# Optimization experiments

Hardware: AMD Instinct MI355X
Metric: run time of the kernel (lower is better)

Reference implementation:

```python
import jax, jax.numpy as jnp
import numpy as np

DIM = 512
HEADS = 8
WIN = 10      # window_size
SHIFT = 5     # shift_size
FRAMES = 1000 # num_frames (N)
HIDDEN = 4 * DIM
EPS = 1e-5


def _layernorm(x, w, b):
    m = jnp.mean(x, axis=-1, keepdims=True)
    v = jnp.mean((x - m) ** 2, axis=-1, keepdims=True)
    return (x - m) * jax.lax.rsqrt(v + EPS) * w + b


def _shift_mask(N):
    pos = jnp.arange(N)
    seg = (pos >= N - WIN).astype(jnp.float32) + (pos >= N - SHIFT).astype(jnp.float32)
    seg = seg.reshape(N // WIN, WIN)
    diff = seg[:, :, None] - seg[:, None, :]
    return jnp.where(diff != 0, -100.0, 0.0)


def setup_inputs() -> dict:
    key = jax.random.key(0)
    ks = jax.random.split(key, 16)
    std = 0.02
    inp = {
        "x": jax.random.normal(ks[0], (64, FRAMES, DIM), dtype=jnp.float32),
        "norm1_w": jnp.ones((DIM,), jnp.float32),
        "norm1_b": jnp.zeros((DIM,), jnp.float32),
        "qkv_w": jax.random.normal(ks[1], (3 * DIM, DIM), jnp.float32) * std,
        "qkv_b": jnp.zeros((3 * DIM,), jnp.float32),
        "rel_bias_table": jax.random.normal(ks[2], (2 * WIN - 1, HEADS), jnp.float32) * std,
        "proj_w": jax.random.normal(ks[3], (DIM, DIM), jnp.float32) * std,
        "proj_b": jnp.zeros((DIM,), jnp.float32),
        "norm2_w": jnp.ones((DIM,), jnp.float32),
        "norm2_b": jnp.zeros((DIM,), jnp.float32),
        "fc1_w": jax.random.normal(ks[4], (HIDDEN, DIM), jnp.float32) * std,
        "fc1_b": jnp.zeros((HIDDEN,), jnp.float32),
        "fc2_w": jax.random.normal(ks[5], (DIM, HIDDEN), jnp.float32) * std,
        "fc2_b": jnp.zeros((DIM,), jnp.float32),
    }
    return inp


def reference(x, norm1_w, norm1_b, qkv_w, qkv_b, rel_bias_table, proj_w, proj_b,
              norm2_w, norm2_b, fc1_w, fc1_b, fc2_w, fc2_b):
    B, N, C = x.shape
    hd = C // HEADS
    scale = hd ** -0.5
    nW = N // WIN

    shortcut = x
    h = _layernorm(x, norm1_w, norm1_b)
    h = jnp.roll(h, -SHIFT, axis=1)                      # cyclic shift
    xw = h.reshape(B * nW, WIN, C)                       # window partition

    qkv = xw @ qkv_w.T + qkv_b
    qkv = qkv.reshape(B * nW, WIN, 3, HEADS, hd).transpose(2, 0, 3, 1, 4)
    q, k, v = qkv[0] * scale, qkv[1], qkv[2]

    attn = jnp.einsum('bhqd,bhkd->bhqk', q, k)
    idx = jnp.arange(WIN)[:, None] - jnp.arange(WIN)[None, :] + WIN - 1
    bias = rel_bias_table[idx]
    attn = attn + bias.transpose(2, 0, 1)[None]

    mask = _shift_mask(N)
    attn = attn.reshape(B, nW, HEADS, WIN, WIN) + mask[None, :, None]
    attn = jax.nn.softmax(attn, axis=-1).reshape(B * nW, HEADS, WIN, WIN)

    out = jnp.einsum('bhqk,bhkd->bhqd', attn, v)
    out = out.transpose(0, 2, 1, 3).reshape(B * nW, WIN, C)
    out = out @ proj_w.T + proj_b

    out = out.reshape(B, N, C)                           # window reverse
    out = jnp.roll(out, SHIFT, axis=1)                   # reverse shift

    x = shortcut + out
    h2 = _layernorm(x, norm2_w, norm2_b)
    h2 = jax.nn.gelu(h2 @ fc1_w.T + fc1_b, approximate=False)
    h2 = h2 @ fc2_w.T + fc2_b
    return x + h2
```

## Files before the change

kernel.cpp:

```cpp
#include <hip/hip_runtime.h>

#define DIMC 512
#define HEADS 8
#define HD 64
#define WINS 10
#define SHIFT_SZ 5
#define FRAMES 1000
#define NWIN 100
#define BATCH 64
#define TOKENS 64000
#define HIDDEN 2048

typedef unsigned short u16;
typedef __attribute__((ext_vector_type(8))) short bf16x8;
typedef __attribute__((ext_vector_type(4))) float f32x4;

__device__ __forceinline__ float bf2f(u16 u) { return __uint_as_float(((unsigned)u) << 16); }
__device__ __forceinline__ u16 f2bf(float f) {
    unsigned u = __float_as_uint(f);
    u += 0x7fffu + ((u >> 16) & 1u);
    return (u16)(u >> 16);
}

__global__ __launch_bounds__(256) void cvt_kernel(const float* __restrict__ src,
                                                  u16* __restrict__ dst, int n) {
    const int i = (blockIdx.x * 256 + threadIdx.x) * 4;
    if (i < n) {
        const float4 v = *(const float4*)(src + i);
        *(ushort4*)(dst + i) = make_ushort4(f2bf(v.x), f2bf(v.y), f2bf(v.z), f2bf(v.w));
    }
}

template <int SH>
__global__ __launch_bounds__(256) void ln_kernel(const float* __restrict__ x,
                                                 const float* __restrict__ w,
                                                 const float* __restrict__ b,
                                                 u16* __restrict__ out) {
    const int wave = threadIdx.x >> 6, lane = threadIdx.x & 63;
    const int row = blockIdx.x * 4 + wave;
    const float4* rp = (const float4*)(x + (size_t)row * DIMC);
    const float4 v0 = rp[lane];
    const float4 v1 = rp[64 + lane];
    float f[8] = {v0.x, v0.y, v0.z, v0.w, v1.x, v1.y, v1.z, v1.w};
    float sum = 0.f, sq = 0.f;
#pragma unroll
    for (int i = 0; i < 8; i++) { sum += f[i]; sq += f[i] * f[i]; }
#pragma unroll
    for (int off = 32; off >= 1; off >>= 1) {
        sum += __shfl_xor(sum, off);
        sq += __shfl_xor(sq, off);
    }
    const float mean = sum * (1.f / DIMC);
    const float var = sq * (1.f / DIMC) - mean * mean;
    const float rstd = rsqrtf(var + 1e-5f);

    const float4 w0 = ((const float4*)w)[lane], w1 = ((const float4*)w)[64 + lane];
    const float4 b0 = ((const float4*)b)[lane], b1 = ((const float4*)b)[64 + lane];
    const float wf[8] = {w0.x, w0.y, w0.z, w0.w, w1.x, w1.y, w1.z, w1.w};
    const float bf[8] = {b0.x, b0.y, b0.z, b0.w, b1.x, b1.y, b1.z, b1.w};
    u16 o[8];
#pragma unroll
    for (int i = 0; i < 8; i++) o[i] = f2bf((f[i] - mean) * rstd * wf[i] + bf[i]);

    int dst = row;
    if (SH) {
        int bb = row / FRAMES;
        int t = row - bb * FRAMES;
        int td = t - SH; if (td < 0) td += FRAMES;
        dst = bb * FRAMES + td;
    }
    u16* op = out + (size_t)dst * DIMC;
    *(ushort4*)(op + 4 * lane) = make_ushort4(o[0], o[1], o[2], o[3]);
    *(ushort4*)(op + 256 + 4 * lane) = make_ushort4(o[4], o[5], o[6], o[7]);
}

__global__ __launch_bounds__(256) void ln_kernel_bf(const u16* __restrict__ x,
                                                    const float* __restrict__ w,
                                                    const float* __restrict__ b,
                                                    u16* __restrict__ out) {
    const int wave = threadIdx.x >> 6, lane = threadIdx.x & 63;
    const int row = blockIdx.x * 4 + wave;
    const uint4 v = ((const uint4*)(x + (size_t)row * DIMC))[lane];
    const unsigned uv[4] = {v.x, v.y, v.z, v.w};
    float f[8];
    float sum = 0.f, sq = 0.f;
#pragma unroll
    for (int i = 0; i < 4; i++) {
        float a = __uint_as_float(uv[i] << 16);
        float c = __uint_as_float(uv[i] & 0xffff0000u);
        f[2 * i] = a; f[2 * i + 1] = c;
        sum += a + c; sq += a * a + c * c;
    }
#pragma unroll
    for (int off = 32; off >= 1; off >>= 1) {
        sum += __shfl_xor(sum, off);
        sq += __shfl_xor(sq, off);
    }
    const float mean = sum * (1.f / DIMC);
    const float var = sq * (1.f / DIMC) - mean * mean;
    const float rstd = rsqrtf(var + 1e-5f);

    const float4 w0 = ((const float4*)w)[2 * lane], w1 = ((const float4*)w)[2 * lane + 1];
    const float4 b0 = ((const float4*)b)[2 * lane], b1 = ((const float4*)b)[2 * lane + 1];
    const float wf[8] = {w0.x, w0.y, w0.z, w0.w, w1.x, w1.y, w1.z, w1.w};
    const float bf[8] = {b0.x, b0.y, b0.z, b0.w, b1.x, b1.y, b1.z, b1.w};
    u16 o[8];
#pragma unroll
    for (int i = 0; i < 8; i++) o[i] = f2bf((f[i] - mean) * rstd * wf[i] + bf[i]);
    uint4 ov;
    ov.x = (unsigned)o[0] | ((unsigned)o[1] << 16);
    ov.y = (unsigned)o[2] | ((unsigned)o[3] << 16);
    ov.z = (unsigned)o[4] | ((unsigned)o[5] << 16);
    ov.w = (unsigned)o[6] | ((unsigned)o[7] << 16);
    ((uint4*)(out + (size_t)row * DIMC))[lane] = ov;
}

#define GLD16(gp, lp)                                                                     \
    __builtin_amdgcn_global_load_lds((const __attribute__((address_space(1))) void*)(gp), \
                                     (__attribute__((address_space(3))) void*)(lp), 16, 0, 0)

template <int MODE>
__global__ __launch_bounds__(256, 2) void gemm_bt(const u16* __restrict__ A,
                                                  const u16* __restrict__ W,
                                                  const float* __restrict__ bias,
                                                  u16* __restrict__ Cb,
                                                  float* __restrict__ Cf,
                                                  const float* __restrict__ Rf,
                                                  const u16* __restrict__ Rb,
                                                  int Nn, int K, int nbn) {
    __shared__ __align__(16) u16 smem[36864];
    const int tid = threadIdx.x;
    const int w = tid >> 6, l = tid & 63;

    const int nwg = gridDim.x;
    const int q8 = nwg >> 3, r8 = nwg & 7;
    const int xcd = blockIdx.x & 7, bidx = blockIdx.x >> 3;
    const int swz = (xcd < r8 ? xcd * (q8 + 1) : r8 * (q8 + 1) + (xcd - r8) * q8) + bidx;
    const int bm = swz / nbn, bn = swz - bm * nbn;

    const int wr = w >> 1, wc = w & 1;
    const int lrow = l & 15, lq = l >> 4;

    f32x4 acc[8][4];
#pragma unroll
    for (int m = 0; m < 8; m++)
#pragma unroll
        for (int n = 0; n < 4; n++) acc[m][n] = (f32x4)0.0f;

    const int gsrc8 = (((tid & 3) ^ ((tid >> 3) & 3)) << 3);
    const u16* Ag = A + (size_t)(bm * 256 + (tid >> 2)) * K + gsrc8;
    const u16* Bg = W + (size_t)(bn * 128 + (tid >> 2)) * K + gsrc8;
    const size_t rowoff = (size_t)64 * K;
    const int lb = w * 512;

#define STAGE(buf, kt) do {                                       \
        u16* sb_ = smem + (buf) * 12288;                          \
        GLD16(Ag + (kt), sb_ + lb);                               \
        GLD16(Ag + rowoff + (kt), sb_ + 2048 + lb);               \
        GLD16(Ag + 2 * rowoff + (kt), sb_ + 4096 + lb);           \
        GLD16(Ag + 3 * rowoff + (kt), sb_ + 6144 + lb);           \
        GLD16(Bg + (kt), sb_ + 8192 + lb);                        \
        GLD16(Bg + rowoff + (kt), sb_ + 10240 + lb);              \
    } while (0)

    const int gran = ((lq ^ ((lrow >> 1) & 3)) << 3);
    const int arow = (wr * 128 + lrow) * 32 + gran;
    const int brow = 8192 + (wc * 64 + lrow) * 32 + gran;

#define COMPUTE(buf) do {                                                          \
        const u16* sb = smem + (buf) * 12288;                                      \
        bf16x8 bv[4];                                                              \
        _Pragma("unroll")                                                          \
        for (int n = 0; n < 4; n++) bv[n] = *(const bf16x8*)(sb + brow + n * 512); \
        _Pragma("unroll")                                                          \
        for (int m = 0; m < 8; m++) {                                              \
            const bf16x8 af = *(const bf16x8*)(sb + arow + m * 512);               \
            _Pragma("unroll")                                                      \
            for (int n = 0; n < 4; n++)              \
                acc[m][n] = __builtin_amdgcn_mfma_f32_16x16x32_bf16(bv[n], af, acc[m][n], 0, 0, 0); \
        }                                                                          \
    } while (0)

    const int nt = K >> 5;
    STAGE(0, 0);
    STAGE(1, 32);
    int cb = 0;
    for (int t = 0; t < nt - 1; ++t) {
        asm volatile("s_waitcnt vmcnt(6)" ::: "memory");
        __builtin_amdgcn_s_barrier();
        __builtin_amdgcn_sched_barrier(0);
        COMPUTE(cb);
        if (t + 2 < nt) {
            const int sbuf = cb == 0 ? 2 : cb - 1;
            STAGE(sbuf, (t + 2) * 32);
        }
        cb = cb == 2 ? 0 : cb + 1;
    }
    asm volatile("s_waitcnt vmcnt(0)" ::: "memory");
    __builtin_amdgcn_s_barrier();
    __builtin_amdgcn_sched_barrier(0);
    COMPUTE(cb);

    if (MODE == 0 || MODE == 1 || MODE == 2) {
        __syncthreads();
#pragma unroll
        for (int m = 0; m < 8; m++) {
            const int row = wr * 128 + m * 16 + lrow;
            const int sw = (row & 7) << 3;
#pragma unroll
            for (int n = 0; n < 4; n++) {
                const int col = wc * 64 + n * 16 + lq * 4;
                const float4 b4 = *(const float4*)(bias + bn * 128 + col);
                float v0 = acc[m][n][0] + b4.x, v1 = acc[m][n][1] + b4.y;
                float v2 = acc[m][n][2] + b4.z, v3 = acc[m][n][3] + b4.w;
                if (MODE == 2) {
                    const float g0 = v0 * (0.7978845608f + 0.0356774081f * v0 * v0);
                    const float g1 = v1 * (0.7978845608f + 0.0356774081f * v1 * v1);
                    const float g2 = v2 * (0.7978845608f + 0.0356774081f * v2 * v2);
                    const float g3 = v3 * (0.7978845608f + 0.0356774081f * v3 * v3);
                    v0 /= (1.f + __expf(-2.f * g0)); v1 /= (1.f + __expf(-2.f * g1));
                    v2 /= (1.f + __expf(-2.f * g2)); v3 /= (1.f + __expf(-2.f * g3));
                }
                *(ushort4*)(smem + row * 128 + ((col ^ sw))) =
                    make_ushort4(f2bf(v0), f2bf(v1), f2bf(v2), f2bf(v3));
            }
        }
        __syncthreads();
        const int c8 = lrow * 8;
#pragma unroll
        for (int i = 0; i < 16; i++) {
            const int r = w * 64 + i * 4 + lq;
            const uint4 val = *(const uint4*)(smem + r * 128 + (c8 ^ ((r & 7) << 3)));
            const int grow = bm * 256 + r;
            if (MODE == 1) {
                int bb = grow / FRAMES;
                int tr = grow - bb * FRAMES;
                int td = tr + SHIFT_SZ; if (td >= FRAMES) td -= FRAMES;
                const size_t dr = (size_t)(bb * FRAMES + td) * DIMC + bn * 128 + c8;
                const float4 rA = *(const float4*)(Rf + dr);
                const float4 rB = *(const float4*)(Rf + dr + 4);
                const u16* vp = (const u16*)&val;
                u16 o[8];
                o[0] = f2bf(bf2f(vp[0]) + rA.x); o[1] = f2bf(bf2f(vp[1]) + rA.y);
                o[2] = f2bf(bf2f(vp[2]) + rA.z); o[3] = f2bf(bf2f(vp[3]) + rA.w);
                o[4] = f2bf(bf2f(vp[4]) + rB.x); o[5] = f2bf(bf2f(vp[5]) + rB.y);
                o[6] = f2bf(bf2f(vp[6]) + rB.z); o[7] = f2bf(bf2f(vp[7]) + rB.w);
                uint4 ov;
                ov.x = (unsigned)o[0] | ((unsigned)o[1] << 16);
                ov.y = (unsigned)o[2] | ((unsigned)o[3] << 16);
                ov.z = (unsigned)o[4] | ((unsigned)o[5] << 16);
                ov.w = (unsigned)o[6] | ((unsigned)o[7] << 16);
                *(uint4*)(Cb + dr) = ov;
            } else {
                *(uint4*)(Cb + (size_t)grow * Nn + bn * 128 + c8) = val;
            }
        }
    } else {
#pragma unroll
        for (int m = 0; m < 8; m++) {
            const int grow = bm * 256 + wr * 128 + m * 16 + lrow;
#pragma unroll
            for (int n = 0; n < 4; n++) {
                const int gcb = bn * 128 + wc * 64 + n * 16 + lq * 4;
                const float4 b4 = *(const float4*)(bias + gcb);
                const size_t dr = (size_t)grow * Nn + gcb;
                const ushort4 rb = *(const ushort4*)(Rb + dr);
                float4 o;
                o.x = acc[m][n][0] + b4.x + bf2f(rb.x);
                o.y = acc[m][n][1] + b4.y + bf2f(rb.y);
                o.z = acc[m][n][2] + b4.z + bf2f(rb.z);
                o.w = acc[m][n][3] + b4.w + bf2f(rb.w);
                *(float4*)(Cf + dr) = o;
            }
        }
    }
#undef COMPUTE
#undef STAGE
}

__global__ __launch_bounds__(256) void attn_kernel(const u16* __restrict__ qkv_c,
                                                   const float* __restrict__ relb,
                                                   u16* __restrict__ out,
                                                   int win0) {
    __shared__ __align__(16) u16 kv[WINS * 3 * DIMC];
    __shared__ float S[HEADS][WINS][WINS];
    const int tid = threadIdx.x;
    const int win = win0 + blockIdx.x;
    const u16* src = qkv_c + (size_t)blockIdx.x * (WINS * 3 * DIMC);
    for (int idx = tid * 8; idx < WINS * 3 * DIMC; idx += 2048)
        *(uint4*)(kv + idx) = *(const uint4*)(src + idx);
    __syncthreads();

    const bool lastw = (win % NWIN) == (NWIN - 1);
    for (int e = tid; e < HEADS * WINS * WINS; e += 256) {
        const int hh = e / (WINS * WINS);
        const int rem = e - hh * WINS * WINS;
        const int i = rem / WINS, j = rem - (rem / WINS) * WINS;
        const u16* qp = kv + i * (3 * DIMC) + hh * HD;
        const u16* kp = kv + j * (3 * DIMC) + DIMC + hh * HD;
        float s = 0.f;
#pragma unroll
        for (int c = 0; c < 64; c++) s += bf2f(qp[c]) * bf2f(kp[c]);
        s *= 0.125f;
        s += relb[(i - j + WINS - 1) * HEADS + hh];
        if (lastw && ((i < SHIFT_SZ) != (j < SHIFT_SZ))) s -= 100.f;
        S[hh][i][j] = s;
    }
    __syncthreads();

    if (tid < HEADS * WINS) {
        const int hh = tid / WINS, i = tid - (tid / WINS) * WINS;
        float m = -1e30f;
#pragma unroll
        for (int j = 0; j < WINS; j++) m = fmaxf(m, S[hh][i][j]);
        float e[WINS], sum = 0.f;
#pragma unroll
        for (int j = 0; j < WINS; j++) { e[j] = __expf(S[hh][i][j] - m); sum += e[j]; }
        const float inv = 1.f / sum;
#pragma unroll
        for (int j = 0; j < WINS; j++) S[hh][i][j] = e[j] * inv;
    }
    __syncthreads();

    {
        const int hh = tid >> 5, dl = tid & 31;
#pragma unroll
        for (int half = 0; half < 2; half++) {
            const int d = dl + half * 32;
            float vv[WINS];
#pragma unroll
            for (int j = 0; j < WINS; j++) vv[j] = bf2f(kv[j * (3 * DIMC) + 2 * DIMC + hh * HD + d]);
#pragma unroll
            for (int i = 0; i < WINS; i++) {
                float o = 0.f;
#pragma unroll
                for (int j = 0; j < WINS; j++) o += S[hh][i][j] * vv[j];
                out[(size_t)(win * WINS + i) * DIMC + hh * HD + d] = f2bf(o);
            }
        }
    }
}

extern "C" void kernel_launch(void* const* d_in, const int* in_sizes, int n_in,
                              void* d_out, int out_size, void* d_ws, size_t ws_size,
                              hipStream_t stream) {
    const float* x     = (const float*)d_in[0];
    const float* n1w   = (const float*)d_in[1];
    const float* n1b   = (const float*)d_in[2];
    const float* qkvw  = (const float*)d_in[3];
    const float* qkvb  = (const float*)d_in[4];
    const float* relb  = (const float*)d_in[5];
    const float* projw = (const float*)d_in[6];
    const float* projb = (const float*)d_in[7];
    const float* n2w   = (const float*)d_in[8];
    const float* n2b   = (const float*)d_in[9];
    const float* fc1w  = (const float*)d_in[10];
    const float* fc1b  = (const float*)d_in[11];
    const float* fc2w  = (const float*)d_in[12];
    const float* fc2b  = (const float*)d_in[13];

    float* outp = (float*)d_out;
    char* ws = (char*)d_ws;
    u16* wb_qkv  = (u16*)(ws);
    u16* wb_proj = (u16*)(ws + 1572864);
    u16* wb_fc1  = (u16*)(ws + 2097152);
    u16* wb_fc2  = (u16*)(ws + 4194304);
    u16* r0  = (u16*)(ws + 6291456);
    u16* x2b = (u16*)(ws + 71827456);
    u16* big = (u16*)(ws + 137363456);

    cvt_kernel<<<768, 256, 0, stream>>>(qkvw, wb_qkv, 786432);
    cvt_kernel<<<256, 256, 0, stream>>>(projw, wb_proj, 262144);
    cvt_kernel<<<1024, 256, 0, stream>>>(fc1w, wb_fc1, 1048576);
    cvt_kernel<<<1024, 256, 0, stream>>>(fc2w, wb_fc2, 1048576);

    const size_t avail = ws_size > (size_t)137363456 ? ws_size - (size_t)137363456 : 0;
    const int nc1 = (avail >= (size_t)98304000) ? 2
                  : (avail >= (size_t)39321600) ? 5 : (avail >= (size_t)19660800) ? 10 : 50;
    const int nc2 = (avail >= (size_t)131072000) ? 2
                  : (avail >= (size_t)52428800) ? 5 : (avail >= (size_t)26214400) ? 10 : 25;

    ln_kernel<SHIFT_SZ><<<TOKENS / 4, 256, 0, stream>>>(x, n1w, n1b, r0);

    const int rows1 = TOKENS / nc1;
    for (int c = 0; c < nc1; ++c) {
        const int row0 = c * rows1;
        gemm_bt<0><<<(rows1 / 256) * 12, 256, 0, stream>>>(
            r0 + (size_t)row0 * DIMC, wb_qkv, qkvb, big, nullptr, nullptr, nullptr, 1536, DIMC, 12);
        attn_kernel<<<rows1 / WINS, 256, 0, stream>>>(big, relb, r0, row0 / WINS);
    }

    gemm_bt<1><<<(TOKENS / 256) * 4, 256, 0, stream>>>(
        r0, wb_proj, projb, x2b, nullptr, x, nullptr, DIMC, DIMC, 4);

    ln_kernel_bf<<<TOKENS / 4, 256, 0, stream>>>(x2b, n2w, n2b, r0);

    const int rows2 = TOKENS / nc2;
    for (int c = 0; c < nc2; ++c) {
        const int row0 = c * rows2;
        gemm_bt<2><<<(rows2 / 256) * 16, 256, 0, stream>>>(
            r0 + (size_t)row0 * DIMC, wb_fc1, fc1b, big, nullptr, nullptr, nullptr, HIDDEN, DIMC, 16);
        gemm_bt<3><<<(rows2 / 256) * 4, 256, 0, stream>>>(
            big, wb_fc2, fc2b, nullptr, outp + (size_t)row0 * DIMC, nullptr,
            x2b + (size_t)row0 * DIMC, DIMC, HIDDEN, 4);
    }
}
```

Measured before the change: 767.7 us.

## Replace GEMM with 256x256-tile, 8-wave kernel and split-phase K pipeline

Replaces the 256x128-tile, 4-wave GEMM with a 256x256-tile kernel using 512 threads (8 waves in a 2x4 grid) and a 64-deep K step. The K step is double-buffered and split into four sub-phases, with loads interleaved between MFMA groups and s_setprio raised around the MFMA groups. The larger tile doubles operand reuse per LDS byte and halves redundant A reads. In exchange it uses 128KB of LDS per block, which limits occupancy, and it halves the number of workgroups.

```diff
diff --git a/kernel.cpp b/kernel.cpp
--- a/kernel.cpp
+++ b/kernel.cpp
@@ -120,15 +120,15 @@
                                      (__attribute__((address_space(3))) void*)(lp), 16, 0, 0)
 
 template <int MODE>
-__global__ __launch_bounds__(256, 2) void gemm_bt(const u16* __restrict__ A,
-                                                  const u16* __restrict__ W,
-                                                  const float* __restrict__ bias,
-                                                  u16* __restrict__ Cb,
-                                                  float* __restrict__ Cf,
-                                                  const float* __restrict__ Rf,
-                                                  const u16* __restrict__ Rb,
-                                                  int Nn, int K, int nbn) {
-    __shared__ __align__(16) u16 smem[36864];
+__global__ __launch_bounds__(512, 2) void gemm8(const u16* __restrict__ A,
+                                                const u16* __restrict__ W,
+                                                const float* __restrict__ bias,
+                                                u16* __restrict__ Cb,
+                                                float* __restrict__ Cf,
+                                                const float* __restrict__ Rf,
+                                                const u16* __restrict__ Rb,
+                                                int Nn, int K, int nbn) {
+    __shared__ __align__(16) u16 smem[65536];
     const int tid = threadIdx.x;
     const int w = tid >> 6, l = tid & 63;
 
@@ -138,7 +138,7 @@
     const int swz = (xcd < r8 ? xcd * (q8 + 1) : r8 * (q8 + 1) + (xcd - r8) * q8) + bidx;
     const int bm = swz / nbn, bn = swz - bm * nbn;
 
-    const int wr = w >> 1, wc = w & 1;
+    const int wm = w >> 2, wn = w & 3;
     const int lrow = l & 15, lq = l >> 4;
 
     f32x4 acc[8][4];
@@ -147,70 +147,113 @@
 #pragma unroll
         for (int n = 0; n < 4; n++) acc[m][n] = (f32x4)0.0f;
 
-    const int gsrc8 = (((tid & 3) ^ ((tid >> 3) & 3)) << 3);
-    const u16* Ag = A + (size_t)(bm * 256 + (tid >> 2)) * K + gsrc8;
-    const u16* Bg = W + (size_t)(bn * 128 + (tid >> 2)) * K + gsrc8;
-    const size_t rowoff = (size_t)64 * K;
-    const int lb = w * 512;
-
-#define STAGE(buf, kt) do {                                       \
-        u16* sb_ = smem + (buf) * 12288;                          \
-        GLD16(Ag + (kt), sb_ + lb);                               \
-        GLD16(Ag + rowoff + (kt), sb_ + 2048 + lb);               \
-        GLD16(Ag + 2 * rowoff + (kt), sb_ + 4096 + lb);           \
-        GLD16(Ag + 3 * rowoff + (kt), sb_ + 6144 + lb);           \
-        GLD16(Bg + (kt), sb_ + 8192 + lb);                        \
-        GLD16(Bg + rowoff + (kt), sb_ + 10240 + lb);              \
-    } while (0)
+    const int lgsrc8 = (((tid & 3) ^ ((tid >> 3) & 3)) << 3);
+    const u16* Ag = A + (size_t)(bm * 256 + (tid >> 2)) * K + lgsrc8;
+    const u16* Wg = W + (size_t)(bn * 256 + (tid >> 2)) * K + lgsrc8;
+    const size_t roff = (size_t)128 * K;
+    const int ldsw = w * 512;
+
+#define STG2(base, G, kc) do {                          \
+        GLD16((G) + (kc), smem + (base) + ldsw);        \
+        GLD16((G) + roff + (kc), smem + (base) + 4096 + ldsw); } while (0)
 
     const int gran = ((lq ^ ((lrow >> 1) & 3)) << 3);
-    const int arow = (wr * 128 + lrow) * 32 + gran;
-    const int brow = 8192 + (wc * 64 + lrow) * 32 + gran;
-
-#define COMPUTE(buf) do {                                                          \
-        const u16* sb = smem + (buf) * 12288;                                      \
-        bf16x8 bv[4];                                                              \
-        _Pragma("unroll")                                                          \
-        for (int n = 0; n < 4; n++) bv[n] = *(const bf16x8*)(sb + brow + n * 512); \
-        _Pragma("unroll")                                                          \
-        for (int m = 0; m < 8; m++) {                                              \
-            const bf16x8 af = *(const bf16x8*)(sb + arow + m * 512);               \
-            _Pragma("unroll")                                                      \
-            for (int n = 0; n < 4; n++)              \
-                acc[m][n] = __builtin_amdgcn_mfma_f32_16x16x32_bf16(bv[n], af, acc[m][n], 0, 0, 0); \
-        }                                                                          \
-    } while (0)
-
-    const int nt = K >> 5;
-    STAGE(0, 0);
-    STAGE(1, 32);
-    int cb = 0;
-    for (int t = 0; t < nt - 1; ++t) {
-        asm volatile("s_waitcnt vmcnt(6)" ::: "memory");
+    const int agb = (wm * 128 + lrow) * 32 + gran;
+    const int bgb = (wn * 64 + lrow) * 32 + gran;
+
+    const int NT = K >> 6;
+
+    STG2(0, Ag, 0);
+    STG2(32768, Wg, 0);
+    STG2(8192, Ag, 32);
+    STG2(32768 + 8192, Wg, 32);
+
+    for (int tt = 0; tt < NT; ++tt) {
+        const int buf = tt & 1;
+        const u16* Ab = smem + buf * 16384;
+        const u16* Bb = smem + 32768 + buf * 16384;
+        const int nb = (buf ^ 1) * 16384;
+        const int nk = (tt + 1) << 6;
+        const bool more = (tt + 1) < NT;
+        bf16x8 af[8];
+
+        if (more) STG2(nb, Ag, nk);
+        if (more) asm volatile("s_waitcnt vmcnt(6)" ::: "memory");
+        else      asm volatile("s_waitcnt vmcnt(4)" ::: "memory");
         __builtin_amdgcn_s_barrier();
         __builtin_amdgcn_sched_barrier(0);
-        COMPUTE(cb);
-        if (t + 2 < nt) {
-            const int sbuf = cb == 0 ? 2 : cb - 1;
-            STAGE(sbuf, (t + 2) * 32);
-        }
-        cb = cb == 2 ? 0 : cb + 1;
-    }
-    asm volatile("s_waitcnt vmcnt(0)" ::: "memory");
-    __builtin_amdgcn_s_barrier();
-    __builtin_amdgcn_sched_barrier(0);
-    COMPUTE(cb);
-
-    if (MODE == 0 || MODE == 1 || MODE == 2) {
-        __syncthreads();
+        {
+#pragma unroll
+            for (int m = 0; m < 8; m++) af[m] = *(const bf16x8*)(Ab + agb + m * 512);
+            const bf16x8 b0 = *(const bf16x8*)(Bb + bgb);
+            const bf16x8 b1 = *(const bf16x8*)(Bb + bgb + 512);
+            __builtin_amdgcn_s_setprio(1);
+#pragma unroll
+            for (int m = 0; m < 8; m++) {
+                acc[m][0] = __builtin_amdgcn_mfma_f32_16x16x32_bf16(b0, af[m], acc[m][0], 0, 0, 0);
+                acc[m][1] = __builtin_amdgcn_mfma_f32_16x16x32_bf16(b1, af[m], acc[m][1], 0, 0, 0);
+            }
+            __builtin_amdgcn_s_setprio(0);
+        }
+        if (more) STG2(32768 + nb, Wg, nk);
+        __builtin_amdgcn_s_barrier();
+        __builtin_amdgcn_sched_barrier(0);
+        {
+            const bf16x8 b2 = *(const bf16x8*)(Bb + bgb + 1024);
+            const bf16x8 b3 = *(const bf16x8*)(Bb + bgb + 1536);
+            __builtin_amdgcn_s_setprio(1);
+#pragma unroll
+            for (int m = 0; m < 8; m++) {
+                acc[m][2] = __builtin_amdgcn_mfma_f32_16x16x32_bf16(b2, af[m], acc[m][2], 0, 0, 0);
+                acc[m][3] = __builtin_amdgcn_mfma_f32_16x16x32_bf16(b3, af[m], acc[m][3], 0, 0, 0);
+            }
+            __builtin_amdgcn_s_setprio(0);
+        }
+        if (more) STG2(8192 + nb, Ag, nk + 32);
+        if (more) asm volatile("s_waitcnt vmcnt(6)" ::: "memory");
+        else      asm volatile("s_waitcnt vmcnt(0)" ::: "memory");
+        __builtin_amdgcn_s_barrier();
+        __builtin_amdgcn_sched_barrier(0);
+        {
+#pragma unroll
+            for (int m = 0; m < 8; m++) af[m] = *(const bf16x8*)(Ab + 8192 + agb + m * 512);
+            const bf16x8 b0 = *(const bf16x8*)(Bb + 8192 + bgb);
+            const bf16x8 b1 = *(const bf16x8*)(Bb + 8192 + bgb + 512);
+            __builtin_amdgcn_s_setprio(1);
+#pragma unroll
+            for (int m = 0; m < 8; m++) {
+                acc[m][0] = __builtin_amdgcn_mfma_f32_16x16x32_bf16(b0, af[m], acc[m][0], 0, 0, 0);
+                acc[m][1] = __builtin_amdgcn_mfma_f32_16x16x32_bf16(b1, af[m], acc[m][1], 0, 0, 0);
+            }
+            __builtin_amdgcn_s_setprio(0);
+        }
+        if (more) STG2(32768 + 8192 + nb, Wg, nk + 32);
+        __builtin_amdgcn_s_barrier();
+        __builtin_amdgcn_sched_barrier(0);
+        {
+            const bf16x8 b2 = *(const bf16x8*)(Bb + 8192 + bgb + 1024);
+            const bf16x8 b3 = *(const bf16x8*)(Bb + 8192 + bgb + 1536);
+            __builtin_amdgcn_s_setprio(1);
+#pragma unroll
+            for (int m = 0; m < 8; m++) {
+                acc[m][2] = __builtin_amdgcn_mfma_f32_16x16x32_bf16(b2, af[m], acc[m][2], 0, 0, 0);
+                acc[m][3] = __builtin_amdgcn_mfma_f32_16x16x32_bf16(b3, af[m], acc[m][3], 0, 0, 0);
+            }
+            __builtin_amdgcn_s_setprio(0);
+        }
+    }
+
+    __syncthreads();
+
+    if (MODE != 3) {
 #pragma unroll
         for (int m = 0; m < 8; m++) {
-            const int row = wr * 128 + m * 16 + lrow;
+            const int row = wm * 128 + m * 16 + lrow;
             const int sw = (row & 7) << 3;
 #pragma unroll
             for (int n = 0; n < 4; n++) {
-                const int col = wc * 64 + n * 16 + lq * 4;
-                const float4 b4 = *(const float4*)(bias + bn * 128 + col);
+                const int col = wn * 64 + n * 16 + lq * 4;
+                const float4 b4 = *(const float4*)(bias + bn * 256 + col);
                 float v0 = acc[m][n][0] + b4.x, v1 = acc[m][n][1] + b4.y;
                 float v2 = acc[m][n][2] + b4.z, v3 = acc[m][n][3] + b4.w;
                 if (MODE == 2) {
@@ -221,47 +264,66 @@
                     v0 /= (1.f + __expf(-2.f * g0)); v1 /= (1.f + __expf(-2.f * g1));
                     v2 /= (1.f + __expf(-2.f * g2)); v3 /= (1.f + __expf(-2.f * g3));
                 }
-                *(ushort4*)(smem + row * 128 + ((col ^ sw))) =
+                const int cidx = (((col & 127) ^ sw)) | (col & 128);
+                *(ushort4*)(smem + row * 256 + cidx) =
                     make_ushort4(f2bf(v0), f2bf(v1), f2bf(v2), f2bf(v3));
             }
         }
         __syncthreads();
-        const int c8 = lrow * 8;
-#pragma unroll
-        for (int i = 0; i < 16; i++) {
-            const int r = w * 64 + i * 4 + lq;
-            const uint4 val = *(const uint4*)(smem + r * 128 + (c8 ^ ((r & 7) << 3)));
+#pragma unroll
+        for (int i = 0; i < 8; i++) {
+            const int r = i * 32 + (tid >> 4);
+            const int c0 = (tid & 15) << 4;
+            const int sw = (r & 7) << 3;
+            const int cA = ((c0 & 127) ^ sw) | (c0 & 128);
+            const int cB = (((c0 + 8) & 127) ^ sw) | ((c0 + 8) & 128);
+            const uint4 vA = *(const uint4*)(smem + r * 256 + cA);
+            const uint4 vB = *(const uint4*)(smem + r * 256 + cB);
             const int grow = bm * 256 + r;
             if (MODE == 1) {
                 int bb = grow / FRAMES;
                 int tr = grow - bb * FRAMES;
                 int td = tr + SHIFT_SZ; if (td >= FRAMES) td -= FRAMES;
-                const size_t dr = (size_t)(bb * FRAMES + td) * DIMC + bn * 128 + c8;
-                const float4 rA = *(const float4*)(Rf + dr);
-                const float4 rB = *(const float4*)(Rf + dr + 4);
-                const u16* vp = (const u16*)&val;
-                u16 o[8];
-                o[0] = f2bf(bf2f(vp[0]) + rA.x); o[1] = f2bf(bf2f(vp[1]) + rA.y);
-                o[2] = f2bf(bf2f(vp[2]) + rA.z); o[3] = f2bf(bf2f(vp[3]) + rA.w);
-                o[4] = f2bf(bf2f(vp[4]) + rB.x); o[5] = f2bf(bf2f(vp[5]) + rB.y);
-                o[6] = f2bf(bf2f(vp[6]) + rB.z); o[7] = f2bf(bf2f(vp[7]) + rB.w);
-                uint4 ov;
-                ov.x = (unsigned)o[0] | ((unsigned)o[1] << 16);
-                ov.y = (unsigned)o[2] | ((unsigned)o[3] << 16);
-                ov.z = (unsigned)o[4] | ((unsigned)o[5] << 16);
-                ov.w = (unsigned)o[6] | ((unsigned)o[7] << 16);
-                *(uint4*)(Cb + dr) = ov;
+                const size_t dr = (size_t)(bb * FRAMES + td) * DIMC + bn * 256 + c0;
+                const float4 r0 = *(const float4*)(Rf + dr);
+                const float4 r1 = *(const float4*)(Rf + dr + 4);
+                const float4 r2 = *(const float4*)(Rf + dr + 8);
+                const float4 r3 = *(const float4*)(Rf + dr + 12);
+                const u16* pa = (const u16*)&vA;
+                const u16* pb = (const u16*)&vB;
+                u16 o[16];
+                o[0]  = f2bf(bf2f(pa[0]) + r0.x); o[1]  = f2bf(bf2f(pa[1]) + r0.y);
+                o[2]  = f2bf(bf2f(pa[2]) + r0.z); o[3]  = f2bf(bf2f(pa[3]) + r0.w);
+                o[4]  = f2bf(bf2f(pa[4]) + r1.x); o[5]  = f2bf(bf2f(pa[5]) + r1.y);
+                o[6]  = f2bf(bf2f(pa[6]) + r1.z); o[7]  = f2bf(bf2f(pa[7]) + r1.w);
+                o[8]  = f2bf(bf2f(pb[0]) + r2.x); o[9]  = f2bf(bf2f(pb[1]) + r2.y);
+                o[10] = f2bf(bf2f(pb[2]) + r2.z); o[11] = f2bf(bf2f(pb[3]) + r2.w);
+                o[12] = f2bf(bf2f(pb[4]) + r3.x); o[13] = f2bf(bf2f(pb[5]) + r3.y);
+                o[14] = f2bf(bf2f(pb[6]) + r3.z); o[15] = f2bf(bf2f(pb[7]) + r3.w);
+                uint4 oa, ob;
+                oa.x = (unsigned)o[0] | ((unsigned)o[1] << 16);
+                oa.y = (unsigned)o[2] | ((unsigned)o[3] << 16);
+                oa.z = (unsigned)o[4] | ((unsigned)o[5] << 16);
+                oa.w = (unsigned)o[6] | ((unsigned)o[7] << 16);
+                ob.x = (unsigned)o[8] | ((unsigned)o[9] << 16);
+                ob.y = (unsigned)o[10] | ((unsigned)o[11] << 16);
+                ob.z = (unsigned)o[12] | ((unsigned)o[13] << 16);
+                ob.w = (unsigned)o[14] | ((unsigned)o[15] << 16);
+                *(uint4*)(Cb + dr) = oa;
+                *(uint4*)(Cb + dr + 8) = ob;
             } else {
-                *(uint4*)(Cb + (size_t)grow * Nn + bn * 128 + c8) = val;
+                u16* dst = Cb + (size_t)grow * Nn + bn * 256 + c0;
+                *(uint4*)dst = vA;
+                *(uint4*)(dst + 8) = vB;
             }
         }
     } else {
 #pragma unroll
         for (int m = 0; m < 8; m++) {
-            const int grow = bm * 256 + wr * 128 + m * 16 + lrow;
+            const int grow = bm * 256 + wm * 128 + m * 16 + lrow;
 #pragma unroll
             for (int n = 0; n < 4; n++) {
-                const int gcb = bn * 128 + wc * 64 + n * 16 + lq * 4;
+                const int gcb = bn * 256 + wn * 64 + n * 16 + lq * 4;
                 const float4 b4 = *(const float4*)(bias + gcb);
                 const size_t dr = (size_t)grow * Nn + gcb;
                 const ushort4 rb = *(const ushort4*)(Rb + dr);
@@ -274,8 +336,7 @@
             }
         }
     }
-#undef COMPUTE
-#undef STAGE
+#undef STG2
 }
 
 __global__ __launch_bounds__(256) void attn_kernel(const u16* __restrict__ qkv_c,
@@ -385,23 +446,23 @@
     const int rows1 = TOKENS / nc1;
     for (int c = 0; c < nc1; ++c) {
         const int row0 = c * rows1;
-        gemm_bt<0><<<(rows1 / 256) * 12, 256, 0, stream>>>(
-            r0 + (size_t)row0 * DIMC, wb_qkv, qkvb, big, nullptr, nullptr, nullptr, 1536, DIMC, 12);
+        gemm8<0><<<(rows1 / 256) * 6, 512, 0, stream>>>(
+            r0 + (size_t)row0 * DIMC, wb_qkv, qkvb, big, nullptr, nullptr, nullptr, 1536, DIMC, 6);
         attn_kernel<<<rows1 / WINS, 256, 0, stream>>>(big, relb, r0, row0 / WINS);
     }
 
-    gemm_bt<1><<<(TOKENS / 256) * 4, 256, 0, stream>>>(
-        r0, wb_proj, projb, x2b, nullptr, x, nullptr, DIMC, DIMC, 4);
+    gemm8<1><<<(TOKENS / 256) * 2, 512, 0, stream>>>(
+        r0, wb_proj, projb, x2b, nullptr, x, nullptr, DIMC, DIMC, 2);
 
     ln_kernel_bf<<<TOKENS / 4, 256, 0, stream>>>(x2b, n2w, n2b, r0);
 
     const int rows2 = TOKENS / nc2;
     for (int c = 0; c < nc2; ++c) {
         const int row0 = c * rows2;
-        gemm_bt<2><<<(rows2 / 256) * 16, 256, 0, stream>>>(
-            r0 + (size_t)row0 * DIMC, wb_fc1, fc1b, big, nullptr, nullptr, nullptr, HIDDEN, DIMC, 16);
-        gemm_bt<3><<<(rows2 / 256) * 4, 256, 0, stream>>>(
+        gemm8<2><<<(rows2 / 256) * 8, 512, 0, stream>>>(
+            r0 + (size_t)row0 * DIMC, wb_fc1, fc1b, big, nullptr, nullptr, nullptr, HIDDEN, DIMC, 8);
+        gemm8<3><<<(rows2 / 256) * 2, 512, 0, stream>>>(
             big, wb_fc2, fc2b, nullptr, outp + (size_t)row0 * DIMC, nullptr,
-            x2b + (size_t)row0 * DIMC, DIMC, HIDDEN, 4);
-    }
-}
+            x2b + (size_t)row0 * DIMC, DIMC, HIDDEN, 2);
+    }
+}
```

Result: slower. 805.4 us (+4.9%).
